# Performance work log

Hardware: AMD Instinct MI355X
Metric: run time of the kernel (lower is better)

## Reference

```python
import jax, jax.numpy as jnp
import numpy as np

B, C, H, W = 4, 512, 32, 32
HEADS, HD = 8, 64          # head_dim = C // heads
SEQ, CTX = 77, 768
GROUPS = 8
EPS = 1e-5


def group_norm(x, w, b):
    # x: [B,C,H,W], normalize per group over (C//G, H, W)
    Bs, Cs, Hs, Ws = x.shape
    xg = x.reshape(Bs, GROUPS, Cs // GROUPS, Hs, Ws)
    mu = xg.mean(axis=(2, 3, 4), keepdims=True)
    var = xg.var(axis=(2, 3, 4), keepdims=True)
    xg = (xg - mu) * jax.lax.rsqrt(var + EPS)
    x = xg.reshape(Bs, Cs, Hs, Ws)
    return x * w[None, :, None, None] + b[None, :, None, None]


def conv1x1(x, w, b):
    # x: [B,C,H,W], w: [O,C], b: [O]
    return jnp.einsum('bchw,oc->bohw', x, w) + b[None, :, None, None]


def attn_core(q, k, v):
    # q: [B,h,Nq,d], k/v: [B,h,Nk,d]
    scale = 1.0 / jnp.sqrt(jnp.asarray(HD, q.dtype))
    scores = jnp.einsum('bhqd,bhkd->bhqk', q, k) * scale
    p = jax.nn.softmax(scores, axis=-1)
    return jnp.einsum('bhqk,bhkd->bhqd', p, v)


def setup_inputs() -> dict:
    key = jax.random.key(0)
    ks = jax.random.split(key, 24)
    s = lambda i, shape, fan: (jax.random.normal(ks[i], shape, jnp.float32)
                               * (1.0 / np.sqrt(fan)))
    return {
        'x': jax.random.normal(ks[0], (B, C, H, W), jnp.float32),
        'context': jax.random.normal(ks[1], (B, SEQ, CTX), jnp.float32),
        # self-attention
        'sa_norm_w': jnp.ones((C,), jnp.float32),
        'sa_norm_b': jnp.zeros((C,), jnp.float32),
        'sa_qkv_w': s(2, (3 * C, C), C), 'sa_qkv_b': jnp.zeros((3 * C,), jnp.float32),
        'sa_proj_w': s(3, (C, C), C), 'sa_proj_b': jnp.zeros((C,), jnp.float32),
        # cross-attention
        'ca_norm_w': jnp.ones((C,), jnp.float32),
        'ca_norm_b': jnp.zeros((C,), jnp.float32),
        'ca_q_w': s(4, (C, C), C), 'ca_q_b': jnp.zeros((C,), jnp.float32),
        'ca_kv_w': s(5, (2 * C, CTX), CTX), 'ca_kv_b': jnp.zeros((2 * C,), jnp.float32),
        'ca_proj_w': s(6, (C, C), C), 'ca_proj_b': jnp.zeros((C,), jnp.float32),
        # FFN
        'ffn_norm_w': jnp.ones((C,), jnp.float32),
        'ffn_norm_b': jnp.zeros((C,), jnp.float32),
        'ffn_w1': s(7, (4 * C, C), C), 'ffn_b1': jnp.zeros((4 * C,), jnp.float32),
        'ffn_w2': s(8, (C, 4 * C), 4 * C), 'ffn_b2': jnp.zeros((C,), jnp.float32),
    }


def reference(x, context,
              sa_norm_w, sa_norm_b, sa_qkv_w, sa_qkv_b, sa_proj_w, sa_proj_b,
              ca_norm_w, ca_norm_b, ca_q_w, ca_q_b, ca_kv_w, ca_kv_b,
              ca_proj_w, ca_proj_b,
              ffn_norm_w, ffn_norm_b, ffn_w1, ffn_b1, ffn_w2, ffn_b2):
    Bs, Cs, Hs, Ws = x.shape
    N = Hs * Ws

    # ---- self-attention (dropout=0 / eval) ----
    h = group_norm(x, sa_norm_w, sa_norm_b)
    qkv = conv1x1(h, sa_qkv_w, sa_qkv_b)                      # [B,3C,H,W]
    q, k, v = jnp.split(qkv, 3, axis=1)
    def to_heads(t):  # [B,C,H,W] -> [B,heads,N,hd]
        return t.reshape(Bs, HEADS, HD, N).transpose(0, 1, 3, 2)
    out = attn_core(to_heads(q), to_heads(k), to_heads(v))    # [B,h,N,d]
    out = out.transpose(0, 1, 3, 2).reshape(Bs, Cs, Hs, Ws)
    x = x + conv1x1(out, sa_proj_w, sa_proj_b)

    # ---- cross-attention ----
    h = group_norm(x, ca_norm_w, ca_norm_b)
    q = conv1x1(h, ca_q_w, ca_q_b)
    q = q.reshape(Bs, HEADS, HD, N).transpose(0, 1, 3, 2)     # [B,h,N,d]
    kv = jnp.einsum('bsc,oc->bso', context, ca_kv_w) + ca_kv_b  # [B,S,2C]
    kv = kv.reshape(Bs, SEQ, 2, HEADS, HD)
    k = kv[:, :, 0].transpose(0, 2, 1, 3)                     # [B,h,S,d]
    v = kv[:, :, 1].transpose(0, 2, 1, 3)
    out = attn_core(q, k, v)                                  # [B,h,N,d]
    out = out.transpose(0, 1, 3, 2).reshape(Bs, Cs, Hs, Ws)
    x = x + conv1x1(out, ca_proj_w, ca_proj_b)

    # ---- FFN: GroupNorm -> conv1x1(4C) -> GELU(exact) -> conv1x1(C) ----
    h = group_norm(x, ffn_norm_w, ffn_norm_b)
    h = conv1x1(h, ffn_w1, ffn_b1)
    h = jax.nn.gelu(h, approximate=False)
    h = conv1x1(h, ffn_w2, ffn_b2)
    return x + h
```

## Files before the change

### kernel.cpp

```cpp
#include <hip/hip_runtime.h>

#define TPB 256
#define Bsz 4
#define Nsp 1024
#define Cch 512
#define SEQ 77
#define CTX 768
#define EPSV 1e-5f
#define MTOK 4096
#define SCL_L2E 0.18033688011111834f

typedef __attribute__((ext_vector_type(8))) short s8v;
typedef __attribute__((ext_vector_type(4))) float f32x4;
typedef const __attribute__((address_space(1))) void* gas_t;
typedef __attribute__((address_space(3))) void* las_t;

static __device__ __forceinline__ float bf2f(short s) {
  union { unsigned u; float f; } z; z.u = ((unsigned)(unsigned short)s) << 16; return z.f;
}
static __device__ __forceinline__ short f2bf(float f) {
  union { float f; unsigned u; } v; v.f = f;
  unsigned r = v.u + 0x7fffu + ((v.u >> 16) & 1u);
  return (short)(r >> 16);
}

__global__ __launch_bounds__(TPB) void prep(const float* a0, const float* a1,
                                            const float* a2, const float* a3,
                                            const float* a4, const float* a5,
                                            const float* a6, short* __restrict__ wdst,
                                            const float* __restrict__ ctx,
                                            short* __restrict__ cdst,
                                            const float* __restrict__ x,
                                            float2* __restrict__ statsPart,
                                            float2* __restrict__ statsCA,
                                            float2* __restrict__ statsFFN) {
  int blk = blockIdx.x;
  int tid = threadIdx.x;
  if (blk < 4352) {
    int u = blk * TPB + tid;
    const float* src; int base;
    if      (u < 196608) { src = a0; base = 0; }
    else if (u < 262144) { src = a1; base = 196608; }
    else if (u < 327680) { src = a2; base = 262144; }
    else if (u < 524288) { src = a3; base = 327680; }
    else if (u < 589824) { src = a4; base = 524288; }
    else if (u < 851968) { src = a5; base = 589824; }
    else                 { src = a6; base = 851968; }
    float4 v = *(const float4*)(src + (size_t)(u - base) * 4);
    short4 o = make_short4(f2bf(v.x), f2bf(v.y), f2bf(v.z), f2bf(v.w));
    *(short4*)(wdst + (size_t)u * 4) = o;
    return;
  }
  if (blk < 4640) {
    int u = (blk - 4352) * TPB + tid;
    int row = u / 192, c4 = u - row * 192;
    int b = row / 96, s_ = row - b * 96;
    short4 o;
    if (s_ < SEQ) {
      float4 v = *(const float4*)(ctx + ((size_t)(b * SEQ + s_)) * CTX + c4 * 4);
      o = make_short4(f2bf(v.x), f2bf(v.y), f2bf(v.z), f2bf(v.w));
    } else {
      o = make_short4(0, 0, 0, 0);
    }
    *(short4*)(cdst + (size_t)row * CTX + c4 * 4) = o;
    return;
  }
  int idx = blk - 4640;
  int bg = idx >> 3, part = idx & 7;
  const float* base = x + (size_t)bg * 65536 + part * 8192;
  float s = 0.f, s2 = 0.f;
#pragma unroll
  for (int it = 0; it < 8; ++it) {
    float4 v = ((const float4*)base)[it * 256 + tid];
    s += v.x + v.y + v.z + v.w;
    s2 += v.x * v.x + v.y * v.y + v.z * v.z + v.w * v.w;
  }
  for (int off = 1; off < 64; off <<= 1) {
    s += __shfl_xor(s, off, 64);
    s2 += __shfl_xor(s2, off, 64);
  }
  __shared__ float red[2][4];
  int wid = tid >> 6;
  if ((tid & 63) == 0) { red[0][wid] = s; red[1][wid] = s2; }
  __syncthreads();
  if (tid == 0) {
    float S = red[0][0] + red[0][1] + red[0][2] + red[0][3];
    float S2 = red[1][0] + red[1][1] + red[1][2] + red[1][3];
    statsPart[idx] = make_float2(S, S2);
  } else if (tid == 1 && part == 0) {
    statsCA[bg] = make_float2(0.f, 0.f);
  } else if (tid == 2 && part == 0) {
    statsFFN[bg] = make_float2(0.f, 0.f);
  }
}

__global__ __launch_bounds__(TPB) void gn_apply(const float* __restrict__ x,
                                                const float* __restrict__ w,
                                                const float* __restrict__ bb,
                                                const float2* __restrict__ stats,
                                                short* __restrict__ outp,
                                                int npart) {
  int t = blockIdx.x, bg = blockIdx.y;
  int b = bg >> 3, g = bg & 7;
  float S = 0.f, S2 = 0.f;
  for (int p = 0; p < npart; ++p) {
    float2 st = stats[bg * npart + p];
    S += st.x; S2 += st.y;
  }
  const float inv = 1.f / 65536.f;
  float mu = S * inv;
  float var = S2 * inv - mu * mu;
  float rstd = rsqrtf(var + EPSV);
  __shared__ float tile[64][65];
  int tid = threadIdx.x;
  int n0 = t * 64;
  const float* p = x + (size_t)bg * 65536;
#pragma unroll
  for (int it = 0; it < 4; ++it) {
    int idx = it * 256 + tid;
    int c = idx >> 4, n4 = (idx & 15) * 4;
    float4 v = *(const float4*)(p + (size_t)c * 1024 + n0 + n4);
    float wc = w[g * 64 + c] * rstd;
    float bc = bb[g * 64 + c] - mu * wc;
    tile[c][n4 + 0] = v.x * wc + bc;
    tile[c][n4 + 1] = v.y * wc + bc;
    tile[c][n4 + 2] = v.z * wc + bc;
    tile[c][n4 + 3] = v.w * wc + bc;
  }
  __syncthreads();
  int n = tid >> 2, cs = (tid & 3) * 16;
  short ob[16];
#pragma unroll
  for (int j = 0; j < 16; ++j) ob[j] = f2bf(tile[cs + j][n]);
  short* op = outp + (size_t)(b * 1024 + n0 + n) * 512 + g * 64 + cs;
  *(int4*)op = *(int4*)&ob[0];
  *(int4*)(op + 8) = *(int4*)&ob[8];
}

template<int BM, int BN, int MODE>
__global__ __launch_bounds__(TPB) void gemm_nt(const short* __restrict__ A,
                                               const short* __restrict__ Bw,
                                               const float* __restrict__ bias,
                                               const float* __restrict__ resid,
                                               void* __restrict__ outp,
                                               short* __restrict__ tout,
                                               int tstride, int K, int O,
                                               float oscale,
                                               float2* __restrict__ stats_out) {
  const int FM = BM / 32, FN = BN / 32;
  __shared__ __align__(16) short As[BM * 64];
  __shared__ __align__(16) short Bs[BN * 64];
  int tid = threadIdx.x;
  int lane = tid & 63, w = tid >> 6;
  int wr = w >> 1, wc = w & 1;
  int m0 = blockIdx.x * BM, o0 = blockIdx.y * BN;
  f32x4 acc[FM][FN];
#pragma unroll
  for (int i = 0; i < FM; ++i)
#pragma unroll
    for (int j = 0; j < FN; ++j) acc[i][j] = (f32x4){0.f, 0.f, 0.f, 0.f};
  int nk = K >> 6;
  for (int kt = 0; kt < nk; ++kt) {
    int k0 = kt << 6;
    __syncthreads();
#pragma unroll
    for (int i = 0; i < BM / 32; ++i) {
      int c = i * 256 + tid;
      int r = c >> 3, qs = c & 7, qg = qs ^ (r & 7);
      const char* ga = (const char*)(A + ((size_t)(m0 + r) * K + k0)) + (qg << 4);
      __builtin_amdgcn_global_load_lds((gas_t)ga, (las_t)((char*)As + (c << 4)), 16, 0, 0);
    }
#pragma unroll
    for (int i = 0; i < BN / 32; ++i) {
      int c = i * 256 + tid;
      int r = c >> 3, qs = c & 7, qg = qs ^ (r & 7);
      const char* gb = (const char*)(Bw + ((size_t)(o0 + r) * K + k0)) + (qg << 4);
      __builtin_amdgcn_global_load_lds((gas_t)gb, (las_t)((char*)Bs + (c << 4)), 16, 0, 0);
    }
    __syncthreads();
#pragma unroll
    for (int kk = 0; kk < 2; ++kk) {
      s8v a[FM], bfr[FN];
#pragma unroll
      for (int m = 0; m < FM; ++m) {
        int r = wr * (BM / 2) + m * 16 + (lane & 15);
        int q = (lane >> 4) + (kk << 2);
        a[m] = *(const s8v*)((const char*)As + r * 128 + ((q ^ (r & 7)) << 4));
      }
#pragma unroll
      for (int n = 0; n < FN; ++n) {
        int r = wc * (BN / 2) + n * 16 + (lane & 15);
        int q = (lane >> 4) + (kk << 2);
        bfr[n] = *(const s8v*)((const char*)Bs + r * 128 + ((q ^ (r & 7)) << 4));
      }
#pragma unroll
      for (int m = 0; m < FM; ++m)
#pragma unroll
        for (int n = 0; n < FN; ++n)
          acc[m][n] = __builtin_amdgcn_mfma_f32_16x16x32_bf16(a[m], bfr[n], acc[m][n], 0, 0, 0);
    }
  }
  float bv[FN];
#pragma unroll
  for (int n = 0; n < FN; ++n) bv[n] = bias[o0 + wc * (BN / 2) + n * 16 + (lane & 15)];
  int row_b = m0 + wr * (BM / 2) + ((lane >> 4) << 2);
  int col_b = o0 + wc * (BN / 2) + (lane & 15);
  const int split = (MODE == 3) ? 1024 : 512;
  if ((MODE == 3 || MODE == 4) && o0 >= split) {
#pragma unroll
    for (int m = 0; m < FM; ++m) {
#pragma unroll
      for (int n = 0; n < FN; ++n) {
        int og = col_b + n * 16;
        short4 s4 = make_short4(f2bf(acc[m][n][0] + bv[n]), f2bf(acc[m][n][1] + bv[n]),
                                f2bf(acc[m][n][2] + bv[n]), f2bf(acc[m][n][3] + bv[n]));
        *(short4*)(tout + (size_t)(og - split) * tstride + row_b + m * 16) = s4;
      }
    }
    return;
  }
  if (MODE == 1) {
    float ls = 0.f, ls2 = 0.f;
#pragma unroll
    for (int m = 0; m < FM; ++m) {
      int t0 = row_b + m * 16;
      int b = t0 >> 10, n_ = t0 & 1023;
#pragma unroll
      for (int n = 0; n < FN; ++n) {
        int og = col_b + n * 16;
        size_t idx = ((size_t)(b * O + og)) * 1024 + n_;
        float4 rv = *(const float4*)(resid + idx);
        float4 ov;
        ov.x = acc[m][n][0] + bv[n] + rv.x;
        ov.y = acc[m][n][1] + bv[n] + rv.y;
        ov.z = acc[m][n][2] + bv[n] + rv.z;
        ov.w = acc[m][n][3] + bv[n] + rv.w;
        *(float4*)((float*)outp + idx) = ov;
        ls += ov.x + ov.y + ov.z + ov.w;
        ls2 += ov.x * ov.x + ov.y * ov.y + ov.z * ov.z + ov.w * ov.w;
      }
    }
    if (stats_out != nullptr) {
      float s = ls, s2 = ls2;
      for (int off = 1; off < 64; off <<= 1) {
        s += __shfl_xor(s, off, 64);
        s2 += __shfl_xor(s2, off, 64);
      }
      __syncthreads();
      float* red = (float*)As;
      if (lane == 0) { red[w * 2] = s; red[w * 2 + 1] = s2; }
      __syncthreads();
      if (tid == 0) {
        float S = red[0] + red[2] + red[4] + red[6];
        float S2 = red[1] + red[3] + red[5] + red[7];
        int bg = (m0 >> 10) * 8 + (o0 >> 6);
        atomicAdd((float*)stats_out + bg * 2, S);
        atomicAdd((float*)stats_out + bg * 2 + 1, S2);
      }
    }
    return;
  }
#pragma unroll
  for (int m = 0; m < FM; ++m) {
#pragma unroll
    for (int i = 0; i < 4; ++i) {
      int mg = row_b + m * 16 + i;
#pragma unroll
      for (int n = 0; n < FN; ++n) {
        int og = col_b + n * 16;
        float v = acc[m][n][i] + bv[n];
        size_t idx = (size_t)mg * O + og;
        if (MODE == 2) {
          float gv = 0.5f * v * (1.f + erff(v * 0.70710678118654752f));
          ((short*)outp)[idx] = f2bf(gv);
        } else if (MODE == 3) {
          if (og < 512) v *= SCL_L2E;
          ((short*)outp)[idx] = f2bf(v);
        } else if (MODE == 0) {
          ((short*)outp)[idx] = f2bf(v * oscale);
        } else {
          ((short*)outp)[idx] = f2bf(v);
        }
      }
    }
  }
}

__global__ __launch_bounds__(TPB) void sa_attn_mfma(const short* __restrict__ qkv,
                                                    const short* __restrict__ vt,
                                                    short* __restrict__ outp) {
  __shared__ __align__(16) short Ks[2][128 * 64];
  __shared__ __align__(16) short Vs[2][64 * 128];
  __shared__ __align__(16) short Ps[4][16 * 128];
  int b = blockIdx.z, h = blockIdx.y, q0 = blockIdx.x * 64;
  int tid = threadIdx.x, lane = tid & 63, w = tid >> 6;
  int g = lane >> 4, qi = lane & 15;
  s8v qf[2];
  {
    const short* qp = qkv + (size_t)(b * 1024 + q0 + w * 16 + qi) * 1536 + h * 64 + g * 8;
    qf[0] = *(const s8v*)qp;
    qf[1] = *(const s8v*)(qp + 32);
  }
  f32x4 o[4];
#pragma unroll
  for (int d = 0; d < 4; ++d) o[d] = (f32x4){0.f, 0.f, 0.f, 0.f};
  float mrun = -1e30f, lrun = 0.f;
  const short* kbase = qkv + (size_t)(b * 1024) * 1536 + 512 + h * 64;
  const short* vbase = vt + (size_t)(h * 64) * 4096 + b * 1024;
  char* psw = (char*)Ps + w * 4096;
  int pswz = (qi & 15) << 4;

  auto stage = [&](int bufi, int kt) {
    int k0 = kt * 128;
#pragma unroll
    for (int i = 0; i < 4; ++i) {
      int c = i * 256 + tid;
      int r = c >> 3, cs = c & 7, cg = cs ^ (r & 7);
      const char* gp = (const char*)(kbase + (size_t)(k0 + r) * 1536) + (cg << 4);
      __builtin_amdgcn_global_load_lds((gas_t)gp, (las_t)((char*)Ks[bufi] + (c << 4)), 16, 0, 0);
    }
#pragma unroll
    for (int i = 0; i < 4; ++i) {
      int c = i * 256 + tid;
      int r = c >> 4, cs = c & 15, cg = cs ^ (r & 15);
      const char* gp = (const char*)(vbase + (size_t)r * 4096 + k0) + (cg << 4);
      __builtin_amdgcn_global_load_lds((gas_t)gp, (las_t)((char*)Vs[bufi] + (c << 4)), 16, 0, 0);
    }
  };

  stage(0, 0);
  __syncthreads();
  for (int kt = 0; kt < 8; ++kt) {
    int cur = kt & 1;
    if (kt < 7) stage(cur ^ 1, kt + 1);
    f32x4 st[8];
#pragma unroll
    for (int t = 0; t < 8; ++t) st[t] = (f32x4){0.f, 0.f, 0.f, 0.f};
#pragma unroll
    for (int s = 0; s < 2; ++s) {
#pragma unroll
      for (int t = 0; t < 8; ++t) {
        int r = t * 16 + qi;
        s8v kf = *(const s8v*)((const char*)Ks[cur] + r * 128 + (((s * 4 + g) ^ (r & 7)) << 4));
        st[t] = __builtin_amdgcn_mfma_f32_16x16x32_bf16(kf, qf[s], st[t], 0, 0, 0);
      }
    }
    float sv[32];
#pragma unroll
    for (int t = 0; t < 8; ++t)
#pragma unroll
      for (int r2 = 0; r2 < 4; ++r2) sv[t * 4 + r2] = st[t][r2];
    float mx = sv[0];
#pragma unroll
    for (int i = 1; i < 32; ++i) mx = fmaxf(mx, sv[i]);
    mx = fmaxf(mx, __shfl_xor(mx, 16));
    mx = fmaxf(mx, __shfl_xor(mx, 32));
    float mnew = fmaxf(mrun, mx);
    float psum = 0.f;
#pragma unroll
    for (int i = 0; i < 32; ++i) { sv[i] = exp2f(sv[i] - mnew); psum += sv[i]; }
    psum += __shfl_xor(psum, 16);
    psum += __shfl_xor(psum, 32);
    float scale = exp2f(mrun - mnew);
    lrun = lrun * scale + psum;
    mrun = mnew;
#pragma unroll
    for (int d = 0; d < 4; ++d) o[d] *= scale;
#pragma unroll
    for (int t = 0; t < 8; ++t) {
      short4 pk = make_short4(f2bf(sv[t * 4]), f2bf(sv[t * 4 + 1]),
                              f2bf(sv[t * 4 + 2]), f2bf(sv[t * 4 + 3]));
      *(short4*)(psw + qi * 256 + ((t * 32 + g * 8) ^ pswz)) = pk;
    }
#pragma unroll
    for (int s = 0; s < 4; ++s) {
      s8v bf = *(const s8v*)(psw + qi * 256 + ((s * 64 + g * 16) ^ pswz));
#pragma unroll
      for (int d = 0; d < 4; ++d) {
        int r = d * 16 + qi;
        s8v af = *(const s8v*)((const char*)Vs[cur] + r * 256 + (((s * 4 + g) ^ (r & 15)) << 4));
        o[d] = __builtin_amdgcn_mfma_f32_16x16x32_bf16(af, bf, o[d], 0, 0, 0);
      }
    }
    __syncthreads();
  }
  float rl = 1.f / lrun;
  short* ob = outp + (size_t)(b * 1024 + q0 + w * 16 + qi) * 512 + h * 64;
#pragma unroll
  for (int d = 0; d < 4; ++d) {
    short4 s4 = make_short4(f2bf(o[d][0] * rl), f2bf(o[d][1] * rl),
                            f2bf(o[d][2] * rl), f2bf(o[d][3] * rl));
    *(short4*)(ob + d * 16 + g * 4) = s4;
  }
}

__global__ __launch_bounds__(TPB) void ca_attn_mfma(const short* __restrict__ qb,
                                                    const short* __restrict__ kvb,
                                                    const short* __restrict__ cavt,
                                                    short* __restrict__ outp) {
  __shared__ __align__(16) short Ks[96 * 64];
  __shared__ __align__(16) short Vs[64 * 128];
  __shared__ __align__(16) short Ps[4][16 * 128];
  int b = blockIdx.z, h = blockIdx.y, q0 = blockIdx.x * 64;
  int tid = threadIdx.x, lane = tid & 63, w = tid >> 6;
  int g = lane >> 4, qi = lane & 15;
  s8v qf[2];
  {
    const short* qp = qb + (size_t)(b * 1024 + q0 + w * 16 + qi) * 512 + h * 64 + g * 8;
    qf[0] = *(const s8v*)qp;
    qf[1] = *(const s8v*)(qp + 32);
  }
  const short* kbase = kvb + (size_t)(b * 96) * 1024 + h * 64;
#pragma unroll
  for (int i = 0; i < 3; ++i) {
    int c = i * 256 + tid;
    int r = c >> 3, cs = c & 7, cg = cs ^ (r & 7);
    const char* gp = (const char*)(kbase + (size_t)r * 1024) + (cg << 4);
    __builtin_amdgcn_global_load_lds((gas_t)gp, (las_t)((char*)Ks + (c << 4)), 16, 0, 0);
  }
#pragma unroll
  for (int i = 0; i < 3; ++i) {
    int c = i * 256 + tid;
    int r = c / 12, jj = c - r * 12;
    int4 dv = *(const int4*)(cavt + (size_t)(h * 64 + r) * 384 + b * 96 + jj * 8);
    *(int4*)((char*)Vs + r * 256 + ((jj * 16) ^ ((r & 7) << 4))) = dv;
  }
  __syncthreads();
  f32x4 st[6];
#pragma unroll
  for (int t = 0; t < 6; ++t) st[t] = (f32x4){0.f, 0.f, 0.f, 0.f};
#pragma unroll
  for (int s = 0; s < 2; ++s) {
#pragma unroll
    for (int t = 0; t < 6; ++t) {
      int r = t * 16 + qi;
      s8v kf = *(const s8v*)((const char*)Ks + r * 128 + (((s * 4 + g) ^ (r & 7)) << 4));
      st[t] = __builtin_amdgcn_mfma_f32_16x16x32_bf16(kf, qf[s], st[t], 0, 0, 0);
    }
  }
  float sv[24];
#pragma unroll
  for (int t = 0; t < 6; ++t)
#pragma unroll
    for (int r2 = 0; r2 < 4; ++r2) {
      int key = t * 16 + g * 4 + r2;
      sv[t * 4 + r2] = (key < SEQ) ? st[t][r2] : -1e30f;
    }
  float mx = sv[0];
#pragma unroll
  for (int i = 1; i < 24; ++i) mx = fmaxf(mx, sv[i]);
  mx = fmaxf(mx, __shfl_xor(mx, 16));
  mx = fmaxf(mx, __shfl_xor(mx, 32));
  float l = 0.f;
#pragma unroll
  for (int i = 0; i < 24; ++i) { sv[i] = exp2f(sv[i] - mx); l += sv[i]; }
  l += __shfl_xor(l, 16);
  l += __shfl_xor(l, 32);
  char* psw = (char*)Ps + w * 4096;
  int pswz = (qi & 7) << 4;
#pragma unroll
  for (int t = 0; t < 6; ++t) {
    short4 pk = make_short4(f2bf(sv[t * 4]), f2bf(sv[t * 4 + 1]),
                            f2bf(sv[t * 4 + 2]), f2bf(sv[t * 4 + 3]));
    *(short4*)(psw + qi * 256 + ((t * 32 + g * 8) ^ pswz)) = pk;
  }
  f32x4 o[4];
#pragma unroll
  for (int d = 0; d < 4; ++d) o[d] = (f32x4){0.f, 0.f, 0.f, 0.f};
#pragma unroll
  for (int s = 0; s < 3; ++s) {
    s8v bf = *(const s8v*)(psw + qi * 256 + ((s * 64 + g * 16) ^ pswz));
#pragma unroll
    for (int d = 0; d < 4; ++d) {
      int r = d * 16 + qi;
      s8v af = *(const s8v*)((const char*)Vs + r * 256 + (((s * 64 + g * 16) ^ ((r & 7) << 4))));
      o[d] = __builtin_amdgcn_mfma_f32_16x16x32_bf16(af, bf, o[d], 0, 0, 0);
    }
  }
  float rl = 1.f / l;
  short* ob = outp + (size_t)(b * 1024 + q0 + w * 16 + qi) * 512 + h * 64;
#pragma unroll
  for (int d = 0; d < 4; ++d) {
    short4 s4 = make_short4(f2bf(o[d][0] * rl), f2bf(o[d][1] * rl),
                            f2bf(o[d][2] * rl), f2bf(o[d][3] * rl));
    *(short4*)(ob + d * 16 + g * 4) = s4;
  }
}

extern "C" void kernel_launch(void* const* d_in, const int* in_sizes, int n_in,
                              void* d_out, int out_size, void* d_ws, size_t ws_size,
                              hipStream_t stream) {
  const float* x        = (const float*)d_in[0];
  const float* context  = (const float*)d_in[1];
  const float* sa_nw    = (const float*)d_in[2];
  const float* sa_nb    = (const float*)d_in[3];
  const float* sa_qkv_w = (const float*)d_in[4];
  const float* sa_qkv_b = (const float*)d_in[5];
  const float* sa_pw    = (const float*)d_in[6];
  const float* sa_pb    = (const float*)d_in[7];
  const float* ca_nw    = (const float*)d_in[8];
  const float* ca_nb    = (const float*)d_in[9];
  const float* ca_qw    = (const float*)d_in[10];
  const float* ca_qb    = (const float*)d_in[11];
  const float* ca_kvw   = (const float*)d_in[12];
  const float* ca_kvb   = (const float*)d_in[13];
  const float* ca_pw    = (const float*)d_in[14];
  const float* ca_pb    = (const float*)d_in[15];
  const float* ff_nw    = (const float*)d_in[16];
  const float* ff_nb    = (const float*)d_in[17];
  const float* ff_w1    = (const float*)d_in[18];
  const float* ff_b1    = (const float*)d_in[19];
  const float* ff_w2    = (const float*)d_in[20];
  const float* ff_b2    = (const float*)d_in[21];
  float* outp = (float*)d_out;

  char* ws = (char*)d_ws;
  float*  xcur  = (float*)(ws);
  short*  hb    = (short*)(ws + (8u << 20));
  short*  big   = (short*)(ws + (12u << 20));
  short*  qkvb  = big;
  short*  qb    = big;
  short*  h1    = big;
  short*  vt    = (short*)(ws + (28u << 20));
  short*  kvb   = (short*)(ws + (32u << 20));
  short*  cavt  = (short*)(ws + (33u << 20));
  short*  ctxb  = (short*)(ws + (34u << 20));
  float2* statsPart = (float2*)(ws + (35u << 20));
  float2* statsCA   = statsPart + 256;
  float2* statsFFN  = statsPart + 288;
  short*  wb    = (short*)(ws + (36u << 20));

  short* w_qkv = wb;
  short* w_sap = wb + 786432;
  short* w_caq = wb + 1048576;
  short* w_kv  = wb + 1310720;
  short* w_cap = wb + 2097152;
  short* w_f1  = wb + 2359296;
  short* w_f2  = wb + 3407872;

  dim3 blk(TPB);
  prep<<<4896, blk, 0, stream>>>(sa_qkv_w, sa_pw, ca_qw, ca_kvw, ca_pw, ff_w1, ff_w2, wb,
                                 context, ctxb, x, statsPart, statsCA, statsFFN);

  gn_apply<<<dim3(16, 32), blk, 0, stream>>>(x, sa_nw, sa_nb, statsPart, hb, 8);
  gemm_nt<128, 128, 3><<<dim3(32, 12), blk, 0, stream>>>(hb, w_qkv, sa_qkv_b, nullptr, qkvb, vt, 4096, 512, 1536, 1.f, nullptr);
  sa_attn_mfma<<<dim3(16, 8, 4), blk, 0, stream>>>(qkvb, vt, hb);
  gemm_nt<128, 64, 1><<<dim3(32, 8), blk, 0, stream>>>(hb, w_sap, sa_pb, x, xcur, nullptr, 0, 512, 512, 1.f, statsCA);

  gn_apply<<<dim3(16, 32), blk, 0, stream>>>(xcur, ca_nw, ca_nb, statsCA, hb, 1);
  gemm_nt<128, 64, 0><<<dim3(32, 8), blk, 0, stream>>>(hb, w_caq, ca_qb, nullptr, qb, nullptr, 0, 512, 512, SCL_L2E, nullptr);
  gemm_nt<64, 64, 4><<<dim3(6, 16), blk, 0, stream>>>(ctxb, w_kv, ca_kvb, nullptr, kvb, cavt, 384, 768, 1024, 1.f, nullptr);
  ca_attn_mfma<<<dim3(16, 8, 4), blk, 0, stream>>>(qb, kvb, cavt, hb);
  gemm_nt<128, 64, 1><<<dim3(32, 8), blk, 0, stream>>>(hb, w_cap, ca_pb, xcur, xcur, nullptr, 0, 512, 512, 1.f, statsFFN);

  gn_apply<<<dim3(16, 32), blk, 0, stream>>>(xcur, ff_nw, ff_nb, statsFFN, hb, 1);
  gemm_nt<128, 128, 2><<<dim3(32, 16), blk, 0, stream>>>(hb, w_f1, ff_b1, nullptr, h1, nullptr, 0, 512, 2048, 1.f, nullptr);
  gemm_nt<128, 64, 1><<<dim3(32, 8), blk, 0, stream>>>(h1, w_f2, ff_b2, xcur, outp, nullptr, 0, 2048, 512, 1.f, nullptr);
}
```

Before: 175.9 us.

## Merge QKV and context KV GEMMs, add lazy softmax rescale and MFMA priority

A new kernel runs the self-attention QKV projection and the cross-attention context KV projection in one launch of 408 blocks, so the KV GEMM no longer needs its own small-grid launch. The self-attention online softmax now rescales the running max and accumulators only when any lane's new max exceeds the old one by more than 11. MFMA sections in both attention kernels are wrapped in s_setprio to favour matrix issue. The bf16 conversion now uses the HIP intrinsic instead of manual rounding. The KV tiles change from 64x64 to 128x128; with only 384 context rows, that gives 24 KV blocks, and the longer K=768 loop makes them the slowest blocks in the merged grid.

```diff
diff --git a/kernel.cpp b/kernel.cpp
--- a/kernel.cpp
+++ b/kernel.cpp
@@ -1,4 +1,5 @@
 #include <hip/hip_runtime.h>
+#include <hip/hip_bf16.h>
 
 #define TPB 256
 #define Bsz 4
@@ -19,9 +20,9 @@
   union { unsigned u; float f; } z; z.u = ((unsigned)(unsigned short)s) << 16; return z.f;
 }
 static __device__ __forceinline__ short f2bf(float f) {
-  union { float f; unsigned u; } v; v.f = f;
-  unsigned r = v.u + 0x7fffu + ((v.u >> 16) & 1u);
-  return (short)(r >> 16);
+  union { __hip_bfloat16 h; short s; } u;
+  u.h = __float2bfloat16(f);
+  return u.s;
 }
 
 __global__ __launch_bounds__(TPB) void prep(const float* a0, const float* a1,
@@ -143,8 +144,7 @@
                                                const float* __restrict__ bias,
                                                const float* __restrict__ resid,
                                                void* __restrict__ outp,
-                                               short* __restrict__ tout,
-                                               int tstride, int K, int O,
+                                               int K, int O,
                                                float oscale,
                                                float2* __restrict__ stats_out) {
   const int FM = BM / 32, FN = BN / 32;
@@ -205,20 +205,6 @@
   for (int n = 0; n < FN; ++n) bv[n] = bias[o0 + wc * (BN / 2) + n * 16 + (lane & 15)];
   int row_b = m0 + wr * (BM / 2) + ((lane >> 4) << 2);
   int col_b = o0 + wc * (BN / 2) + (lane & 15);
-  const int split = (MODE == 3) ? 1024 : 512;
-  if ((MODE == 3 || MODE == 4) && o0 >= split) {
-#pragma unroll
-    for (int m = 0; m < FM; ++m) {
-#pragma unroll
-      for (int n = 0; n < FN; ++n) {
-        int og = col_b + n * 16;
-        short4 s4 = make_short4(f2bf(acc[m][n][0] + bv[n]), f2bf(acc[m][n][1] + bv[n]),
-                                f2bf(acc[m][n][2] + bv[n]), f2bf(acc[m][n][3] + bv[n]));
-        *(short4*)(tout + (size_t)(og - split) * tstride + row_b + m * 16) = s4;
-      }
-    }
-    return;
-  }
   if (MODE == 1) {
     float ls = 0.f, ls2 = 0.f;
 #pragma unroll
@@ -273,14 +259,113 @@
         if (MODE == 2) {
           float gv = 0.5f * v * (1.f + erff(v * 0.70710678118654752f));
           ((short*)outp)[idx] = f2bf(gv);
-        } else if (MODE == 3) {
-          if (og < 512) v *= SCL_L2E;
-          ((short*)outp)[idx] = f2bf(v);
-        } else if (MODE == 0) {
+        } else {
           ((short*)outp)[idx] = f2bf(v * oscale);
-        } else {
-          ((short*)outp)[idx] = f2bf(v);
         }
+      }
+    }
+  }
+}
+
+__global__ __launch_bounds__(TPB) void gemm_qkvkv(
+    const short* __restrict__ hb, const short* __restrict__ wqkv, const float* __restrict__ bqkv,
+    const short* __restrict__ ctxb, const short* __restrict__ wkv, const float* __restrict__ bkv,
+    short* __restrict__ qkvb, short* __restrict__ vt,
+    short* __restrict__ kvb, short* __restrict__ cavt) {
+  __shared__ __align__(16) short As[128 * 64];
+  __shared__ __align__(16) short Bs[128 * 64];
+  int bid = blockIdx.x;
+  const short *A, *Bw; const float* bias;
+  short *outp, *tout;
+  int K, O, m0, o0, split, tstride, qsplit;
+  if (bid < 384) {
+    A = hb; Bw = wqkv; bias = bqkv; outp = qkvb; tout = vt;
+    K = 512; O = 1536; split = 1024; tstride = 4096; qsplit = 512;
+    m0 = (bid & 31) * 128; o0 = (bid >> 5) * 128;
+  } else {
+    int idx = bid - 384;
+    A = ctxb; Bw = wkv; bias = bkv; outp = kvb; tout = cavt;
+    K = 768; O = 1024; split = 512; tstride = 384; qsplit = 0;
+    m0 = (idx % 3) * 128; o0 = (idx / 3) * 128;
+  }
+  int tid = threadIdx.x;
+  int lane = tid & 63, w = tid >> 6;
+  int wr = w >> 1, wc = w & 1;
+  f32x4 acc[4][4];
+#pragma unroll
+  for (int i = 0; i < 4; ++i)
+#pragma unroll
+    for (int j = 0; j < 4; ++j) acc[i][j] = (f32x4){0.f, 0.f, 0.f, 0.f};
+  int nk = K >> 6;
+  for (int kt = 0; kt < nk; ++kt) {
+    int k0 = kt << 6;
+    __syncthreads();
+#pragma unroll
+    for (int i = 0; i < 4; ++i) {
+      int c = i * 256 + tid;
+      int r = c >> 3, qs = c & 7, qg = qs ^ (r & 7);
+      const char* ga = (const char*)(A + ((size_t)(m0 + r) * K + k0)) + (qg << 4);
+      __builtin_amdgcn_global_load_lds((gas_t)ga, (las_t)((char*)As + (c << 4)), 16, 0, 0);
+    }
+#pragma unroll
+    for (int i = 0; i < 4; ++i) {
+      int c = i * 256 + tid;
+      int r = c >> 3, qs = c & 7, qg = qs ^ (r & 7);
+      const char* gb = (const char*)(Bw + ((size_t)(o0 + r) * K + k0)) + (qg << 4);
+      __builtin_amdgcn_global_load_lds((gas_t)gb, (las_t)((char*)Bs + (c << 4)), 16, 0, 0);
+    }
+    __syncthreads();
+#pragma unroll
+    for (int kk = 0; kk < 2; ++kk) {
+      s8v a[4], bfr[4];
+#pragma unroll
+      for (int m = 0; m < 4; ++m) {
+        int r = wr * 64 + m * 16 + (lane & 15);
+        int q = (lane >> 4) + (kk << 2);
+        a[m] = *(const s8v*)((const char*)As + r * 128 + ((q ^ (r & 7)) << 4));
+      }
+#pragma unroll
+      for (int n = 0; n < 4; ++n) {
+        int r = wc * 64 + n * 16 + (lane & 15);
+        int q = (lane >> 4) + (kk << 2);
+        bfr[n] = *(const s8v*)((const char*)Bs + r * 128 + ((q ^ (r & 7)) << 4));
+      }
+#pragma unroll
+      for (int m = 0; m < 4; ++m)
+#pragma unroll
+        for (int n = 0; n < 4; ++n)
+          acc[m][n] = __builtin_amdgcn_mfma_f32_16x16x32_bf16(a[m], bfr[n], acc[m][n], 0, 0, 0);
+    }
+  }
+  float bv[4];
+#pragma unroll
+  for (int n = 0; n < 4; ++n) bv[n] = bias[o0 + wc * 64 + n * 16 + (lane & 15)];
+  int row_b = m0 + wr * 64 + ((lane >> 4) << 2);
+  int col_b = o0 + wc * 64 + (lane & 15);
+  if (o0 >= split) {
+#pragma unroll
+    for (int m = 0; m < 4; ++m) {
+#pragma unroll
+      for (int n = 0; n < 4; ++n) {
+        int og = col_b + n * 16;
+        short4 s4 = make_short4(f2bf(acc[m][n][0] + bv[n]), f2bf(acc[m][n][1] + bv[n]),
+                                f2bf(acc[m][n][2] + bv[n]), f2bf(acc[m][n][3] + bv[n]));
+        *(short4*)(tout + (size_t)(og - split) * tstride + row_b + m * 16) = s4;
+      }
+    }
+    return;
+  }
+#pragma unroll
+  for (int m = 0; m < 4; ++m) {
+#pragma unroll
+    for (int i = 0; i < 4; ++i) {
+      int mg = row_b + m * 16 + i;
+#pragma unroll
+      for (int n = 0; n < 4; ++n) {
+        int og = col_b + n * 16;
+        float v = acc[m][n][i] + bv[n];
+        if (og < qsplit) v *= SCL_L2E;
+        ((short*)outp)[(size_t)mg * O + og] = f2bf(v);
       }
     }
   }
@@ -336,6 +421,7 @@
     f32x4 st[8];
 #pragma unroll
     for (int t = 0; t < 8; ++t) st[t] = (f32x4){0.f, 0.f, 0.f, 0.f};
+    __builtin_amdgcn_s_setprio(1);
 #pragma unroll
     for (int s = 0; s < 2; ++s) {
 #pragma unroll
@@ -345,6 +431,7 @@
         st[t] = __builtin_amdgcn_mfma_f32_16x16x32_bf16(kf, qf[s], st[t], 0, 0, 0);
       }
     }
+    __builtin_amdgcn_s_setprio(0);
     float sv[32];
 #pragma unroll
     for (int t = 0; t < 8; ++t)
@@ -355,23 +442,27 @@
     for (int i = 1; i < 32; ++i) mx = fmaxf(mx, sv[i]);
     mx = fmaxf(mx, __shfl_xor(mx, 16));
     mx = fmaxf(mx, __shfl_xor(mx, 32));
-    float mnew = fmaxf(mrun, mx);
+    if (!__all(mx - mrun <= 11.f)) {
+      float mnew = fmaxf(mrun, mx);
+      float scale = exp2f(mrun - mnew);
+      lrun *= scale;
+#pragma unroll
+      for (int d = 0; d < 4; ++d) o[d] *= scale;
+      mrun = mnew;
+    }
     float psum = 0.f;
 #pragma unroll
-    for (int i = 0; i < 32; ++i) { sv[i] = exp2f(sv[i] - mnew); psum += sv[i]; }
+    for (int i = 0; i < 32; ++i) { sv[i] = exp2f(sv[i] - mrun); psum += sv[i]; }
     psum += __shfl_xor(psum, 16);
     psum += __shfl_xor(psum, 32);
-    float scale = exp2f(mrun - mnew);
-    lrun = lrun * scale + psum;
-    mrun = mnew;
-#pragma unroll
-    for (int d = 0; d < 4; ++d) o[d] *= scale;
+    lrun += psum;
 #pragma unroll
     for (int t = 0; t < 8; ++t) {
       short4 pk = make_short4(f2bf(sv[t * 4]), f2bf(sv[t * 4 + 1]),
                               f2bf(sv[t * 4 + 2]), f2bf(sv[t * 4 + 3]));
       *(short4*)(psw + qi * 256 + ((t * 32 + g * 8) ^ pswz)) = pk;
     }
+    __builtin_amdgcn_s_setprio(1);
 #pragma unroll
     for (int s = 0; s < 4; ++s) {
       s8v bf = *(const s8v*)(psw + qi * 256 + ((s * 64 + g * 16) ^ pswz));
@@ -382,6 +473,7 @@
         o[d] = __builtin_amdgcn_mfma_f32_16x16x32_bf16(af, bf, o[d], 0, 0, 0);
       }
     }
+    __builtin_amdgcn_s_setprio(0);
     __syncthreads();
   }
   float rl = 1.f / lrun;
@@ -429,6 +521,7 @@
   f32x4 st[6];
 #pragma unroll
   for (int t = 0; t < 6; ++t) st[t] = (f32x4){0.f, 0.f, 0.f, 0.f};
+  __builtin_amdgcn_s_setprio(1);
 #pragma unroll
   for (int s = 0; s < 2; ++s) {
 #pragma unroll
@@ -438,6 +531,7 @@
       st[t] = __builtin_amdgcn_mfma_f32_16x16x32_bf16(kf, qf[s], st[t], 0, 0, 0);
     }
   }
+  __builtin_amdgcn_s_setprio(0);
   float sv[24];
 #pragma unroll
   for (int t = 0; t < 6; ++t)
@@ -467,6 +561,7 @@
   f32x4 o[4];
 #pragma unroll
   for (int d = 0; d < 4; ++d) o[d] = (f32x4){0.f, 0.f, 0.f, 0.f};
+  __builtin_amdgcn_s_setprio(1);
 #pragma unroll
   for (int s = 0; s < 3; ++s) {
     s8v bf = *(const s8v*)(psw + qi * 256 + ((s * 64 + g * 16) ^ pswz));
@@ -477,6 +572,7 @@
       o[d] = __builtin_amdgcn_mfma_f32_16x16x32_bf16(af, bf, o[d], 0, 0, 0);
     }
   }
+  __builtin_amdgcn_s_setprio(0);
   float rl = 1.f / l;
   short* ob = outp + (size_t)(b * 1024 + q0 + w * 16 + qi) * 512 + h * 64;
 #pragma unroll
@@ -543,17 +639,17 @@
                                  context, ctxb, x, statsPart, statsCA, statsFFN);
 
   gn_apply<<<dim3(16, 32), blk, 0, stream>>>(x, sa_nw, sa_nb, statsPart, hb, 8);
-  gemm_nt<128, 128, 3><<<dim3(32, 12), blk, 0, stream>>>(hb, w_qkv, sa_qkv_b, nullptr, qkvb, vt, 4096, 512, 1536, 1.f, nullptr);
+  gemm_qkvkv<<<408, blk, 0, stream>>>(hb, w_qkv, sa_qkv_b, ctxb, w_kv, ca_kvb,
+                                      qkvb, vt, kvb, cavt);
   sa_attn_mfma<<<dim3(16, 8, 4), blk, 0, stream>>>(qkvb, vt, hb);
-  gemm_nt<128, 64, 1><<<dim3(32, 8), blk, 0, stream>>>(hb, w_sap, sa_pb, x, xcur, nullptr, 0, 512, 512, 1.f, statsCA);
+  gemm_nt<128, 64, 1><<<dim3(32, 8), blk, 0, stream>>>(hb, w_sap, sa_pb, x, xcur, 512, 512, 1.f, statsCA);
 
   gn_apply<<<dim3(16, 32), blk, 0, stream>>>(xcur, ca_nw, ca_nb, statsCA, hb, 1);
-  gemm_nt<128, 64, 0><<<dim3(32, 8), blk, 0, stream>>>(hb, w_caq, ca_qb, nullptr, qb, nullptr, 0, 512, 512, SCL_L2E, nullptr);
-  gemm_nt<64, 64, 4><<<dim3(6, 16), blk, 0, stream>>>(ctxb, w_kv, ca_kvb, nullptr, kvb, cavt, 384, 768, 1024, 1.f, nullptr);
+  gemm_nt<128, 64, 0><<<dim3(32, 8), blk, 0, stream>>>(hb, w_caq, ca_qb, nullptr, qb, 512, 512, SCL_L2E, nullptr);
   ca_attn_mfma<<<dim3(16, 8, 4), blk, 0, stream>>>(qb, kvb, cavt, hb);
-  gemm_nt<128, 64, 1><<<dim3(32, 8), blk, 0, stream>>>(hb, w_cap, ca_pb, xcur, xcur, nullptr, 0, 512, 512, 1.f, statsFFN);
+  gemm_nt<128, 64, 1><<<dim3(32, 8), blk, 0, stream>>>(hb, w_cap, ca_pb, xcur, xcur, 512, 512, 1.f, statsFFN);
 
   gn_apply<<<dim3(16, 32), blk, 0, stream>>>(xcur, ff_nw, ff_nb, statsFFN, hb, 1);
-  gemm_nt<128, 128, 2><<<dim3(32, 16), blk, 0, stream>>>(hb, w_f1, ff_b1, nullptr, h1, nullptr, 0, 512, 2048, 1.f, nullptr);
-  gemm_nt<128, 64, 1><<<dim3(32, 8), blk, 0, stream>>>(h1, w_f2, ff_b2, xcur, outp, nullptr, 0, 2048, 512, 1.f, nullptr);
-}
+  gemm_nt<128, 128, 2><<<dim3(32, 16), blk, 0, stream>>>(hb, w_f1, ff_b1, nullptr, h1, 512, 2048, 1.f, nullptr);
+  gemm_nt<128, 64, 1><<<dim3(32, 8), blk, 0, stream>>>(h1, w_f2, ff_b2, xcur, outp, 2048, 512, 1.f, nullptr);
+}
```

After: 169.0 us. 3.9% less time.
